# Kernel tuning notes

Measured on AMD Instinct MI355X. Metric: run time of the kernel, lower is better.

Reference implementation:

```python
import jax, jax.numpy as jnp
import numpy as np

PAD = 32      # person_attrs_dim
NZ = 64       # num_zones
T = 32768     # number of timesteps
D = PAD + 1 + NZ  # 97, input dim to the MLP


def _ln(x, g, b, eps=1e-5):
    # LayerNorm over the last (only) axis of a 1-D vector
    m = jnp.mean(x)
    v = jnp.mean((x - m) ** 2)
    return g * (x - m) / jnp.sqrt(v + eps) + b


def setup_inputs() -> dict:
    key = jax.random.key(0)
    ks = jax.random.split(key, 24)

    def xav(k, shape):  # xavier_normal_ for nn.Linear weight [out, in]
        std = np.sqrt(2.0 / (shape[0] + shape[1])).astype(np.float32)
        return std * jax.random.normal(k, shape, dtype=jnp.float32)

    def lng(k, n):  # layernorm gain (perturbed from 1 so grads are non-trivial)
        return 1.0 + 0.1 * jax.random.normal(k, (n,), dtype=jnp.float32)

    def lnb(k, n):
        return 0.1 * jax.random.normal(k, (n,), dtype=jnp.float32)

    inp = {
        "person_attrs": jax.random.normal(ks[0], (PAD,), dtype=jnp.float32),
        "times": jax.random.uniform(ks[1], (T,), dtype=jnp.float32) * 24.0,
        "zone_features": jax.random.normal(ks[2], (NZ, 16), dtype=jnp.float32),
        "edge_index": jax.random.randint(ks[3], (2, 256), 0, NZ, dtype=jnp.int32),
        # input_norm
        "g0": lng(ks[4], D), "b0": lnb(ks[5], D),
        # encoder1: Linear(D,256) + LN(256)
        "W1": xav(ks[6], (256, D)), "b1": jnp.zeros((256,), jnp.float32),
        "g1": lng(ks[7], 256), "be1": lnb(ks[8], 256),
        # encoder2: Linear(256,128) + LN(128)
        "W2": xav(ks[9], (128, 256)), "b2": jnp.zeros((128,), jnp.float32),
        "g2": lng(ks[10], 128), "be2": lnb(ks[11], 128),
        # output_layer: Linear(128,64) + LN(64) + Linear(64,NZ)
        "W3": xav(ks[12], (64, 128)), "b3": jnp.zeros((64,), jnp.float32),
        "g3": lng(ks[13], 64), "be3": lnb(ks[14], 64),
        "W4": xav(ks[15], (NZ, 64)), "b4": jnp.zeros((NZ,), jnp.float32),
    }
    return inp


def reference(person_attrs, times, zone_features, edge_index,
              g0, b0, W1, b1, g1, be1, W2, b2, g2, be2,
              W3, b3, g3, be3, W4, b4):
    nz = W4.shape[0]
    # set_graph_data: symmetric adjacency with self-loops (zone_features unused)
    u, v = edge_index[0], edge_index[1]
    A = jnp.zeros((nz, nz), jnp.float32).at[u, v].set(1.0).at[v, u].set(1.0)
    A = jnp.maximum(A, jnp.eye(nz, dtype=jnp.float32))

    def step(zone, t):
        onehot = jax.nn.one_hot(zone, nz, dtype=jnp.float32)
        x = jnp.concatenate([person_attrs, t[None], onehot])  # [D]
        x = _ln(x, g0, b0)
        h = jax.nn.relu(_ln(W1 @ x + b1, g1, be1))   # dropout is eval-mode identity
        h = jax.nn.relu(_ln(W2 @ h + b2, g2, be2))
        h = jax.nn.relu(_ln(W3 @ h + b3, g3, be3))
        raw = W4 @ h + b4                            # [nz] raw logits
        row = A[zone]
        # (raw/temp with invalid=-50/temp) * temp  ==  where(valid, raw, -50)
        pred = jnp.where(row > 0, raw, jnp.float32(-50.0))
        nxt = jnp.argmax(jnp.where(row > 0, raw, -jnp.inf)).astype(zone.dtype)
        return nxt, pred

    _, zone_logits = jax.lax.scan(step, jnp.array(0, jnp.int32), times)
    return zone_logits  # [T, nz]
```

## Files before the change

### kernel.cpp

```cpp
#include <hip/hip_runtime.h>
#include <stdint.h>

typedef __attribute__((ext_vector_type(8))) short bf16x8;
typedef __attribute__((ext_vector_type(4))) float f32x4;
typedef __attribute__((ext_vector_type(4))) unsigned int u32x4;

#define MFMA(a, b, c) __builtin_amdgcn_mfma_f32_16x16x32_bf16(a, b, c, 0, 0, 0)

__device__ __forceinline__ unsigned short f2b(float x) {
  unsigned u = __float_as_uint(x);
  return (unsigned short)((u + 0x7fffu + ((u >> 16) & 1u)) >> 16);
}
__device__ __forceinline__ float b2f(unsigned short h) {
  return __uint_as_float(((unsigned)h) << 16);
}

struct u2 { unsigned hi, lo; };
__device__ __forceinline__ u2 split2(float h0, float h1) {
  unsigned u0 = __float_as_uint(h0), u1 = __float_as_uint(h1);
  u2 r;
  r.hi = (u0 >> 16) | (u1 & 0xffff0000u);
  float r0 = h0 - __uint_as_float(u0 & 0xffff0000u);
  float r1 = h1 - __uint_as_float(u1 & 0xffff0000u);
  r.lo = (__float_as_uint(r0) >> 16) | (__float_as_uint(r1) & 0xffff0000u);
  return r;
}

#define SWZ(row, col) ((col) ^ ((((row) >> 2) & 1) << 4) ^ ((((row) >> 3) & 1) << 2))


__global__ void k_prep(const float* __restrict__ pa, const float* __restrict__ g0,
                       const float* __restrict__ b0, const float* __restrict__ W1,
                       const float* __restrict__ b1,
                       float* __restrict__ c_pa, float* __restrict__ w_t,
                       float* __restrict__ c_g, float* __restrict__ c_const,
                       float* __restrict__ scal, float* __restrict__ wzT,
                       float* __restrict__ wzZ) {
  int j = threadIdx.x;
  const float* wr = W1 + j * 97;
  float cg = 0.f, cc = 0.f, cp = 0.f;
  for (int k = 0; k < 97; ++k) { float w = wr[k]; cg += w * g0[k]; cc += w * b0[k]; }
  for (int k = 0; k < 32; ++k) cp += wr[k] * g0[k] * pa[k];
  c_g[j] = cg;
  c_const[j] = cc + b1[j];
  c_pa[j] = cp;
  w_t[j] = wr[32] * g0[32];
  for (int z = 0; z < 64; ++z) {
    float v = wr[33 + z] * g0[33 + z];
    wzT[j * 64 + z] = v;
    wzZ[z * 256 + j] = v;
  }
  if (j == 0) {
    float s = 0.f, q = 0.f;
    for (int k = 0; k < 32; ++k) { float x = pa[k]; s += x; q += x * x; }
    scal[0] = s; scal[1] = q;
  }
}

__global__ void k_prep2(const float* __restrict__ c_pa, const float* __restrict__ w_t,
                        const float* __restrict__ c_g, const float* __restrict__ c_const,
                        const float* __restrict__ wzT, float* __restrict__ st) {
  int tid = threadIdx.x;
  if (tid < 64) {
    int z = tid;
    float A = 0.f, Q = 0.f, dpa = 0.f, dwt = 0.f, dcg = 0.f, dcc = 0.f;
    for (int k = 0; k < 256; ++k) {
      float wz = wzT[k * 64 + z];
      A += wz; Q = fmaf(wz, wz, Q);
      dpa = fmaf(c_pa[k], wz, dpa);
      dwt = fmaf(w_t[k], wz, dwt);
      dcg = fmaf(c_g[k], wz, dcg);
      dcc = fmaf(c_const[k], wz, dcc);
    }
    st[z] = A; st[64 + z] = Q; st[128 + z] = dpa;
    st[192 + z] = dwt; st[256 + z] = dcg; st[320 + z] = dcc;
  } else {
    int lane = tid - 64;
    float acc[14];
    #pragma unroll
    for (int m = 0; m < 14; ++m) acc[m] = 0.f;
    for (int k = lane; k < 256; k += 64) {
      float P = c_pa[k], W = w_t[k], G = c_g[k], C = c_const[k];
      acc[0] += P; acc[1] += W; acc[2] += G; acc[3] += C;
      acc[4] = fmaf(P, P, acc[4]); acc[5] = fmaf(P, W, acc[5]);
      acc[6] = fmaf(P, G, acc[6]); acc[7] = fmaf(P, C, acc[7]);
      acc[8] = fmaf(W, W, acc[8]); acc[9] = fmaf(W, G, acc[9]);
      acc[10] = fmaf(W, C, acc[10]); acc[11] = fmaf(G, G, acc[11]);
      acc[12] = fmaf(G, C, acc[12]); acc[13] = fmaf(C, C, acc[13]);
    }
    #pragma unroll
    for (int off = 1; off < 64; off <<= 1) {
      #pragma unroll
      for (int m = 0; m < 14; ++m) acc[m] += __shfl_xor(acc[m], off, 64);
    }
    if (lane == 0) {
      #pragma unroll
      for (int m = 0; m < 14; ++m) st[386 + m] = acc[m];
    }
  }
}

__global__ void k_scal2st(const float* __restrict__ scal, float* __restrict__ st) {
  if (threadIdx.x < 2) st[384 + threadIdx.x] = scal[threadIdx.x];
}

__global__ void k_adj(const int* __restrict__ ei, unsigned long long* __restrict__ adj) {
  int t = threadIdx.x;
  if (t < 64) adj[t] = 1ull << t;
  __syncthreads();
  int u = ei[t] & 63, v = ei[256 + t] & 63;
  atomicOr(&adj[u], 1ull << v);
  atomicOr(&adj[v], 1ull << u);
}

__global__ void k_wsplit(const float* __restrict__ W2, const float* __restrict__ W3,
                         const float* __restrict__ W4,
                         unsigned short* __restrict__ W2Ah, unsigned short* __restrict__ W2Al,
                         unsigned short* __restrict__ W3Ah, unsigned short* __restrict__ W3Al,
                         unsigned short* __restrict__ W4Ah, unsigned short* __restrict__ W4Al) {
  int idx = blockIdx.x * 256 + threadIdx.x;
  float w; unsigned short* ph; unsigned short* pl; int o;
  if (idx < 32768) {
    int mt = idx >> 12, kt = (idx >> 9) & 7, lane = (idx >> 3) & 63, j = idx & 7;
    int m = mt * 16 + (lane & 15), k = kt * 32 + (lane >> 4) * 8 + j;
    w = W2[m * 256 + k]; ph = W2Ah; pl = W2Al; o = idx;
  } else if (idx < 40960) {
    int r = idx - 32768;
    int mt = r >> 11, kt = (r >> 9) & 3, lane = (r >> 3) & 63, j = r & 7;
    int m = mt * 16 + (lane & 15), k = kt * 32 + (lane >> 4) * 8 + j;
    w = W3[m * 128 + k]; ph = W3Ah; pl = W3Al; o = r;
  } else if (idx < 45056) {
    int r = idx - 40960;
    int mt = r >> 10, kt = (r >> 9) & 1, lane = (r >> 3) & 63, j = r & 7;
    int m = mt * 16 + (lane & 15), k = kt * 32 + (lane >> 4) * 8 + j;
    w = W4[m * 64 + k]; ph = W4Ah; pl = W4Al; o = r;
  } else return;
  unsigned short hb = f2b(w);
  ph[o] = hb;
  pl[o] = f2b(w - b2f(hb));
}


__global__ __launch_bounds__(256, 4) void k_pass1(
    const float* __restrict__ times,
    const float* __restrict__ c_pa, const float* __restrict__ w_t,
    const float* __restrict__ c_g, const float* __restrict__ c_const,
    const float* __restrict__ wzT, const float* __restrict__ st,
    const unsigned short* __restrict__ W2Ah, const unsigned short* __restrict__ W2Al,
    const unsigned short* __restrict__ W3Ah, const unsigned short* __restrict__ W3Al,
    const unsigned short* __restrict__ W4Ah, const unsigned short* __restrict__ W4Al,
    const float* __restrict__ b2, const float* __restrict__ b3,
    const float* __restrict__ b4,
    const float* __restrict__ g1, const float* __restrict__ be1,
    const float* __restrict__ g2, const float* __restrict__ be2,
    const float* __restrict__ g3, const float* __restrict__ be3,
    const unsigned long long* __restrict__ adj,
    unsigned char* __restrict__ nxt) {
  __shared__ __align__(16) char region[32768];
  __shared__ float u_lds[256];
  __shared__ float ps1[256], ps2[256];
  __shared__ unsigned long long pk[256];

  unsigned short* B1hi = (unsigned short*)region;
  unsigned short* B1lo = (unsigned short*)(region + 16384);
  float* h2p = (float*)region;
  unsigned short* B2hi = (unsigned short*)region;
  unsigned short* B2lo = (unsigned short*)(region + 16384);
  float* h3p = (float*)region;
  unsigned short* B3hi = (unsigned short*)(region + 16384);
  unsigned short* B3lo = (unsigned short*)(region + 24576);

  const int tid = threadIdx.x;
  const int lane = tid & 63;
  const int l15 = lane & 15;
  const int lhi = lane >> 4;
  const int w = __builtin_amdgcn_readfirstlane(tid >> 6);
  const int i = blockIdx.x;

  const float t = times[i];
  const float m0 = (st[384] + t + 1.0f) * (1.0f / 97.0f);
  const float e2 = (st[385] + t * t + 1.0f) * (1.0f / 97.0f);
  const float alpha = 1.0f / sqrtf(e2 - m0 * m0 + 1e-5f);
  const float gma = -m0 * alpha;

  const f32x4 zero4 = {0.f, 0.f, 0.f, 0.f};

  {
    int k = tid;
    float u = fmaf(t, w_t[k], c_pa[k]);
    u = fmaf(alpha, u, c_const[k]);
    u = fmaf(gma, c_g[k], u);
    u_lds[k] = u;
    float su = u, sq = u * u;
    #pragma unroll
    for (int off = 1; off < 64; off <<= 1) {
      su += __shfl_xor(su, off, 64);
      sq += __shfl_xor(sq, off, 64);
    }
    if (lane == 0) { ps1[w] = su; ps2[w] = sq; }
  }
  __syncthreads();
  float mu1, inv1;
  {
    float U1 = ps1[0] + ps1[1] + ps1[2] + ps1[3];
    float Qu = ps2[0] + ps2[1] + ps2[2] + ps2[3];
    float A1 = st[lane], Qz = st[64 + lane];
    float dpa = st[128 + lane], dwt = st[192 + lane];
    float dcg = st[256 + lane], dcc = st[320 + lane];
    float s1 = fmaf(alpha, A1, U1);
    float uwz = fmaf(alpha, fmaf(t, dwt, dpa), fmaf(gma, dcg, dcc));
    float s2 = Qu + 2.0f * alpha * uwz + alpha * alpha * Qz;
    mu1 = s1 * (1.0f / 256.0f);
    inv1 = 1.0f / sqrtf(s2 * (1.0f / 256.0f) - mu1 * mu1 + 1e-5f);
  }

  f32x4 acc[2][4];
  #pragma unroll
  for (int a = 0; a < 2; ++a)
    #pragma unroll
    for (int b = 0; b < 4; ++b) acc[a][b] = zero4;

  for (int kc = 0; kc < 2; ++kc) {
    if (kc) __syncthreads();
    #pragma unroll
    for (int q = 0; q < 4; ++q) {
      int kb = kc * 128 + w * 32 + q * 8;
      f32x4 u0 = *(const f32x4*)(u_lds + kb);
      f32x4 u1 = *(const f32x4*)(u_lds + kb + 4);
      float hbuf[8];
      #pragma unroll
      for (int j = 0; j < 8; ++j) {
        int k = kb + j;
        float u = (j < 4) ? u0[j] : u1[j - 4];
        float p = fmaf(alpha, wzT[k * 64 + lane], u);
        float gi = g1[k] * inv1;
        float bb = fmaf(-mu1, gi, be1[k]);
        hbuf[j] = fmaxf(fmaf(p, gi, bb), 0.f);
      }
      u32x4 vh, vl;
      #pragma unroll
      for (int e = 0; e < 4; ++e) {
        u2 s = split2(hbuf[2 * e], hbuf[2 * e + 1]);
        vh[e] = s.hi; vl[e] = s.lo;
      }
      int slotd = ((w * 4 + lhi) * 64 + q * 16 + l15) * 4;
      *(u32x4*)((unsigned*)B1hi + slotd) = vh;
      *(u32x4*)((unsigned*)B1lo + slotd) = vl;
    }
    __syncthreads();
    for (int kt = 0; kt < 4; ++kt) {
      int ktg = kc * 4 + kt;
      bf16x8 a0h = *(const bf16x8*)(W2Ah + (((2 * w + 0) * 8 + ktg) * 64 + lane) * 8);
      bf16x8 a0l = *(const bf16x8*)(W2Al + (((2 * w + 0) * 8 + ktg) * 64 + lane) * 8);
      bf16x8 a1h = *(const bf16x8*)(W2Ah + (((2 * w + 1) * 8 + ktg) * 64 + lane) * 8);
      bf16x8 a1l = *(const bf16x8*)(W2Al + (((2 * w + 1) * 8 + ktg) * 64 + lane) * 8);
      #pragma unroll
      for (int nt = 0; nt < 4; ++nt) {
        bf16x8 bh = *(const bf16x8*)(B1hi + ((kt * 4 + nt) * 64 + lane) * 8);
        bf16x8 bl = *(const bf16x8*)(B1lo + ((kt * 4 + nt) * 64 + lane) * 8);
        acc[0][nt] = MFMA(a0h, bh, acc[0][nt]);
        acc[0][nt] = MFMA(a0h, bl, acc[0][nt]);
        acc[0][nt] = MFMA(a0l, bh, acc[0][nt]);
        acc[1][nt] = MFMA(a1h, bh, acc[1][nt]);
        acc[1][nt] = MFMA(a1h, bl, acc[1][nt]);
        acc[1][nt] = MFMA(a1l, bh, acc[1][nt]);
      }
    }
  }
  #pragma unroll
  for (int mti = 0; mti < 2; ++mti) {
    f32x4 bv = *(const f32x4*)(b2 + w * 32 + mti * 16 + lhi * 4);
    #pragma unroll
    for (int nt = 0; nt < 4; ++nt) acc[mti][nt] += bv;
  }
  {
    float sa[4], sb[4];
    #pragma unroll
    for (int nt = 0; nt < 4; ++nt) {
      float x1 = 0.f, x2 = 0.f;
      #pragma unroll
      for (int mti = 0; mti < 2; ++mti)
        #pragma unroll
        for (int r = 0; r < 4; ++r) { float v = acc[mti][nt][r]; x1 += v; x2 += v * v; }
      x1 += __shfl_xor(x1, 16, 64); x1 += __shfl_xor(x1, 32, 64);
      x2 += __shfl_xor(x2, 16, 64); x2 += __shfl_xor(x2, 32, 64);
      sa[nt] = x1; sb[nt] = x2;
    }
    if (lane < 16) {
      #pragma unroll
      for (int nt = 0; nt < 4; ++nt) {
        ps1[w * 64 + nt * 16 + lane] = sa[nt];
        ps2[w * 64 + nt * 16 + lane] = sb[nt];
      }
    }
  }
  __syncthreads();
  #pragma unroll
  for (int mti = 0; mti < 2; ++mti)
    #pragma unroll
    for (int nt = 0; nt < 4; ++nt)
      #pragma unroll
      for (int r = 0; r < 4; ++r) {
        int row = w * 32 + mti * 16 + lhi * 4 + r;
        h2p[row * 64 + SWZ(row, nt * 16 + l15)] = acc[mti][nt][r];
      }
  __syncthreads();

  float mu2, inv2;
  {
    float a = ps1[lane] + ps1[64 + lane] + ps1[128 + lane] + ps1[192 + lane];
    float b = ps2[lane] + ps2[64 + lane] + ps2[128 + lane] + ps2[192 + lane];
    mu2 = a * (1.0f / 128.0f);
    inv2 = 1.0f / sqrtf(b * (1.0f / 128.0f) - mu2 * mu2 + 1e-5f);
  }
  float hv[32];
  #pragma unroll
  for (int mi = 0; mi < 32; ++mi) {
    int row = w * 32 + mi;
    hv[mi] = h2p[row * 64 + SWZ(row, lane)];
  }
  __syncthreads();
  #pragma unroll
  for (int q = 0; q < 4; ++q) {
    float hbuf[8];
    #pragma unroll
    for (int j = 0; j < 8; ++j) {
      int mi = q * 8 + j, mm = w * 32 + mi;
      float gi = g2[mm] * inv2;
      float bb = fmaf(-mu2, gi, be2[mm]);
      hbuf[j] = fmaxf(fmaf(hv[mi], gi, bb), 0.f);
    }
    u32x4 vh, vl;
    #pragma unroll
    for (int e = 0; e < 4; ++e) {
      u2 s = split2(hbuf[2 * e], hbuf[2 * e + 1]);
      vh[e] = s.hi; vl[e] = s.lo;
    }
    int slotd = ((w * 4 + lhi) * 64 + q * 16 + l15) * 4;
    *(u32x4*)((unsigned*)B2hi + slotd) = vh;
    *(u32x4*)((unsigned*)B2lo + slotd) = vl;
  }
  __syncthreads();

  f32x4 acc2[4];
  #pragma unroll
  for (int b = 0; b < 4; ++b) acc2[b] = zero4;
  for (int kt = 0; kt < 4; ++kt) {
    bf16x8 ah = *(const bf16x8*)(W3Ah + ((w * 4 + kt) * 64 + lane) * 8);
    bf16x8 al = *(const bf16x8*)(W3Al + ((w * 4 + kt) * 64 + lane) * 8);
    #pragma unroll
    for (int nt = 0; nt < 4; ++nt) {
      bf16x8 bh = *(const bf16x8*)(B2hi + ((kt * 4 + nt) * 64 + lane) * 8);
      bf16x8 bl = *(const bf16x8*)(B2lo + ((kt * 4 + nt) * 64 + lane) * 8);
      acc2[nt] = MFMA(ah, bh, acc2[nt]);
      acc2[nt] = MFMA(ah, bl, acc2[nt]);
      acc2[nt] = MFMA(al, bh, acc2[nt]);
    }
  }
  {
    f32x4 bv = *(const f32x4*)(b3 + w * 16 + lhi * 4);
    #pragma unroll
    for (int nt = 0; nt < 4; ++nt) acc2[nt] += bv;
  }
  {
    float sa[4], sb[4];
    #pragma unroll
    for (int nt = 0; nt < 4; ++nt) {
      float x1 = 0.f, x2 = 0.f;
      #pragma unroll
      for (int r = 0; r < 4; ++r) { float v = acc2[nt][r]; x1 += v; x2 += v * v; }
      x1 += __shfl_xor(x1, 16, 64); x1 += __shfl_xor(x1, 32, 64);
      x2 += __shfl_xor(x2, 16, 64); x2 += __shfl_xor(x2, 32, 64);
      sa[nt] = x1; sb[nt] = x2;
    }
    if (lane < 16) {
      #pragma unroll
      for (int nt = 0; nt < 4; ++nt) {
        ps1[w * 64 + nt * 16 + lane] = sa[nt];
        ps2[w * 64 + nt * 16 + lane] = sb[nt];
      }
    }
  }
  __syncthreads();
  #pragma unroll
  for (int nt = 0; nt < 4; ++nt)
    #pragma unroll
    for (int r = 0; r < 4; ++r) {
      int row = w * 16 + lhi * 4 + r;
      h3p[row * 64 + SWZ(row, nt * 16 + l15)] = acc2[nt][r];
    }
  __syncthreads();

  float mu3, inv3;
  {
    float a = ps1[lane] + ps1[64 + lane] + ps1[128 + lane] + ps1[192 + lane];
    float b = ps2[lane] + ps2[64 + lane] + ps2[128 + lane] + ps2[192 + lane];
    mu3 = a * (1.0f / 64.0f);
    inv3 = 1.0f / sqrtf(b * (1.0f / 64.0f) - mu3 * mu3 + 1e-5f);
  }
  #pragma unroll
  for (int q = 0; q < 2; ++q) {
    int o = w * 2 + q;
    float hbuf[8];
    #pragma unroll
    for (int j = 0; j < 8; ++j) {
      int mm = o * 8 + j;
      float v = h3p[mm * 64 + SWZ(mm, lane)];
      float gi = g3[mm] * inv3;
      float bb = fmaf(-mu3, gi, be3[mm]);
      hbuf[j] = fmaxf(fmaf(v, gi, bb), 0.f);
    }
    u32x4 vh, vl;
    #pragma unroll
    for (int e = 0; e < 4; ++e) {
      u2 s = split2(hbuf[2 * e], hbuf[2 * e + 1]);
      vh[e] = s.hi; vl[e] = s.lo;
    }
    int slotd = (((o >> 2) * 4 + lhi) * 64 + (o & 3) * 16 + l15) * 4;
    *(u32x4*)((unsigned*)B3hi + slotd) = vh;
    *(u32x4*)((unsigned*)B3lo + slotd) = vl;
  }
  __syncthreads();

  f32x4 acc3[4];
  #pragma unroll
  for (int b = 0; b < 4; ++b) acc3[b] = zero4;
  for (int kt = 0; kt < 2; ++kt) {
    bf16x8 ah = *(const bf16x8*)(W4Ah + ((w * 2 + kt) * 64 + lane) * 8);
    bf16x8 al = *(const bf16x8*)(W4Al + ((w * 2 + kt) * 64 + lane) * 8);
    #pragma unroll
    for (int nt = 0; nt < 4; ++nt) {
      bf16x8 bh = *(const bf16x8*)(B3hi + ((kt * 4 + nt) * 64 + lane) * 8);
      bf16x8 bl = *(const bf16x8*)(B3lo + ((kt * 4 + nt) * 64 + lane) * 8);
      acc3[nt] = MFMA(ah, bh, acc3[nt]);
      acc3[nt] = MFMA(ah, bl, acc3[nt]);
      acc3[nt] = MFMA(al, bh, acc3[nt]);
    }
  }
  f32x4 b4v = *(const f32x4*)(b4 + w * 16 + lhi * 4);
  unsigned long long kbest[4];
  #pragma unroll
  for (int nt = 0; nt < 4; ++nt) {
    unsigned long long am = adj[nt * 16 + l15];
    unsigned long long kb = 0ull;
    #pragma unroll
    for (int r = 0; r < 4; ++r) {
      int o = w * 16 + lhi * 4 + r;
      float raw = acc3[nt][r] + b4v[r];
      float val = ((am >> o) & 1ull) ? raw : -__builtin_huge_valf();
      unsigned u = __float_as_uint(val);
      u = (u & 0x80000000u) ? ~u : (u | 0x80000000u);
      unsigned long long key = ((unsigned long long)u << 6) | (unsigned long long)(63 - o);
      if (key > kb) kb = key;
    }
    unsigned long long oth = __shfl_xor(kb, 16, 64); if (oth > kb) kb = oth;
    oth = __shfl_xor(kb, 32, 64); if (oth > kb) kb = oth;
    kbest[nt] = kb;
  }
  if (lane < 16) {
    #pragma unroll
    for (int nt = 0; nt < 4; ++nt) pk[w * 64 + nt * 16 + lane] = kbest[nt];
  }
  __syncthreads();
  if (tid < 64) {
    unsigned long long k0 = pk[tid], k1 = pk[64 + tid];
    unsigned long long k2 = pk[128 + tid], k3 = pk[192 + tid];
    unsigned long long a = k0 > k1 ? k0 : k1;
    unsigned long long b = k2 > k3 ? k2 : k3;
    unsigned long long bb = a > b ? a : b;
    nxt[(size_t)i * 64 + tid] = (unsigned char)(63u - (unsigned)(bb & 63ull));
  }
}


__global__ void k_scan_a(const unsigned char* __restrict__ nxt,
                         unsigned char* __restrict__ cmap) {
  int c = blockIdx.x, lane = threadIdx.x;
  int g = lane;
  const unsigned char* p = nxt + (size_t)c * 128 * 64;
  for (int s = 0; s < 128; ++s) {
    int sig = p[s * 64 + lane];
    g = __shfl(sig, g, 64);
  }
  cmap[c * 64 + lane] = (unsigned char)g;
}

__global__ void k_scan_b(const unsigned char* __restrict__ cmap,
                         int* __restrict__ startz) {
  int lane = threadIdx.x;
  int cur = 0;
  for (int c = 0; c < 256; ++c) {
    if (lane == 0) startz[c] = cur;
    int row = cmap[c * 64 + lane];
    cur = __shfl(row, cur, 64);
  }
}

__global__ void k_scan_c(const unsigned char* __restrict__ nxt,
                         const int* __restrict__ startz,
                         unsigned char* __restrict__ zones) {
  int c = blockIdx.x, lane = threadIdx.x;
  int cur = startz[c];
  const unsigned char* p = nxt + (size_t)c * 128 * 64;
  for (int s = 0; s < 128; ++s) {
    if (lane == 0) zones[c * 128 + s] = (unsigned char)cur;
    int row = p[s * 64 + lane];
    cur = __shfl(row, cur, 64);
  }
}


__global__ __launch_bounds__(256, 2) void k_pass2m(
    const float* __restrict__ times, const unsigned char* __restrict__ zones,
    const float* __restrict__ c_pa, const float* __restrict__ w_t,
    const float* __restrict__ c_g, const float* __restrict__ c_const,
    const float* __restrict__ wzZ, const float* __restrict__ st,
    const unsigned short* __restrict__ W2Ah, const unsigned short* __restrict__ W2Al,
    const unsigned short* __restrict__ W3Ah, const unsigned short* __restrict__ W3Al,
    const unsigned short* __restrict__ W4Ah, const unsigned short* __restrict__ W4Al,
    const float* __restrict__ b2, const float* __restrict__ b3,
    const float* __restrict__ b4,
    const float* __restrict__ g1, const float* __restrict__ be1,
    const float* __restrict__ g2, const float* __restrict__ be2,
    const float* __restrict__ g3, const float* __restrict__ be3,
    const unsigned long long* __restrict__ adj,
    float* __restrict__ out) {
  __shared__ __align__(16) char region[32768];
  __shared__ float ps1[256], ps2[256];
  __shared__ unsigned long long am_lds[64];

  unsigned short* B1hi = (unsigned short*)region;
  unsigned short* B1lo = (unsigned short*)(region + 16384);
  float* h2p = (float*)region;
  unsigned short* B2hi = (unsigned short*)region;
  unsigned short* B2lo = (unsigned short*)(region + 16384);
  float* h3p = (float*)region;
  unsigned short* B3hi = (unsigned short*)(region + 16384);
  unsigned short* B3lo = (unsigned short*)(region + 24576);
  float* outT = (float*)region;

  const int tid = threadIdx.x;
  const int lane = tid & 63;
  const int l15 = lane & 15;
  const int lhi = lane >> 4;
  const int w = __builtin_amdgcn_readfirstlane(tid >> 6);
  const int i0 = blockIdx.x * 64;

  const float t = times[i0 + lane];
  const int z = zones[i0 + lane];
  const int zrow = z << 8;
  if (tid < 64) am_lds[tid] = adj[zones[i0 + tid]];

  const float m0 = (st[384] + t + 1.0f) * (1.0f / 97.0f);
  const float e2 = (st[385] + t * t + 1.0f) * (1.0f / 97.0f);
  const float a0 = 1.0f / sqrtf(e2 - m0 * m0 + 1e-5f);
  const float a1 = a0 * t;
  const float a2 = -m0 * a0;

  float mu1, inv1;
  {
    float SP = st[386], SW = st[387], SG = st[388], SC = st[389];
    float PP = st[390], PW = st[391], PG = st[392], PC = st[393];
    float WW = st[394], WG = st[395], WC = st[396];
    float GG = st[397], GC = st[398], CC = st[399];
    float U1 = a0 * SP + a1 * SW + a2 * SG + SC;
    float s1 = fmaf(a0, st[z], U1);
    float Qu = a0 * a0 * PP + a1 * a1 * WW + a2 * a2 * GG + CC
             + 2.0f * (a0 * a1 * PW + a0 * a2 * PG + a0 * PC
                       + a1 * a2 * WG + a1 * WC + a2 * GC);
    float uwz = a0 * st[128 + z] + a1 * st[192 + z] + a2 * st[256 + z] + st[320 + z];
    float s2 = Qu + 2.0f * a0 * uwz + a0 * a0 * st[64 + z];
    mu1 = s1 * (1.0f / 256.0f);
    inv1 = 1.0f / sqrtf(s2 * (1.0f / 256.0f) - mu1 * mu1 + 1e-5f);
  }

  const f32x4 zero4 = {0.f, 0.f, 0.f, 0.f};
  f32x4 acc[2][4];
  #pragma unroll
  for (int a = 0; a < 2; ++a)
    #pragma unroll
    for (int b = 0; b < 4; ++b) acc[a][b] = zero4;

  for (int kc = 0; kc < 2; ++kc) {
    if (kc) __syncthreads();
    #pragma unroll
    for (int q = 0; q < 4; ++q) {
      int kb = kc * 128 + w * 32 + q * 8;
      float hbuf[8];
      #pragma unroll
      for (int j = 0; j < 8; ++j) {
        int k = kb + j;
        float u = fmaf(a0, c_pa[k], fmaf(a1, w_t[k], fmaf(a2, c_g[k], c_const[k])));
        float p = fmaf(a0, wzZ[zrow + k], u);
        float gi = g1[k] * inv1;
        float bb = fmaf(-mu1, gi, be1[k]);
        hbuf[j] = fmaxf(fmaf(p, gi, bb), 0.f);
      }
      u32x4 vh, vl;
      #pragma unroll
      for (int e = 0; e < 4; ++e) {
        u2 s = split2(hbuf[2 * e], hbuf[2 * e + 1]);
        vh[e] = s.hi; vl[e] = s.lo;
      }
      int slotd = ((w * 4 + lhi) * 64 + q * 16 + l15) * 4;
      *(u32x4*)((unsigned*)B1hi + slotd) = vh;
      *(u32x4*)((unsigned*)B1lo + slotd) = vl;
    }
    __syncthreads();
    for (int kt = 0; kt < 4; ++kt) {
      int ktg = kc * 4 + kt;
      bf16x8 a0h = *(const bf16x8*)(W2Ah + (((2 * w + 0) * 8 + ktg) * 64 + lane) * 8);
      bf16x8 a0l = *(const bf16x8*)(W2Al + (((2 * w + 0) * 8 + ktg) * 64 + lane) * 8);
      bf16x8 a1h = *(const bf16x8*)(W2Ah + (((2 * w + 1) * 8 + ktg) * 64 + lane) * 8);
      bf16x8 a1l = *(const bf16x8*)(W2Al + (((2 * w + 1) * 8 + ktg) * 64 + lane) * 8);
      #pragma unroll
      for (int nt = 0; nt < 4; ++nt) {
        bf16x8 bh = *(const bf16x8*)(B1hi + ((kt * 4 + nt) * 64 + lane) * 8);
        bf16x8 bl = *(const bf16x8*)(B1lo + ((kt * 4 + nt) * 64 + lane) * 8);
        acc[0][nt] = MFMA(a0h, bh, acc[0][nt]);
        acc[0][nt] = MFMA(a0h, bl, acc[0][nt]);
        acc[0][nt] = MFMA(a0l, bh, acc[0][nt]);
        acc[1][nt] = MFMA(a1h, bh, acc[1][nt]);
        acc[1][nt] = MFMA(a1h, bl, acc[1][nt]);
        acc[1][nt] = MFMA(a1l, bh, acc[1][nt]);
      }
    }
  }
  #pragma unroll
  for (int mti = 0; mti < 2; ++mti) {
    f32x4 bv = *(const f32x4*)(b2 + w * 32 + mti * 16 + lhi * 4);
    #pragma unroll
    for (int nt = 0; nt < 4; ++nt) acc[mti][nt] += bv;
  }
  {
    float sa[4], sb[4];
    #pragma unroll
    for (int nt = 0; nt < 4; ++nt) {
      float x1 = 0.f, x2 = 0.f;
      #pragma unroll
      for (int mti = 0; mti < 2; ++mti)
        #pragma unroll
        for (int r = 0; r < 4; ++r) { float v = acc[mti][nt][r]; x1 += v; x2 += v * v; }
      x1 += __shfl_xor(x1, 16, 64); x1 += __shfl_xor(x1, 32, 64);
      x2 += __shfl_xor(x2, 16, 64); x2 += __shfl_xor(x2, 32, 64);
      sa[nt] = x1; sb[nt] = x2;
    }
    if (lane < 16) {
      #pragma unroll
      for (int nt = 0; nt < 4; ++nt) {
        ps1[w * 64 + nt * 16 + lane] = sa[nt];
        ps2[w * 64 + nt * 16 + lane] = sb[nt];
      }
    }
  }
  __syncthreads();
  #pragma unroll
  for (int mti = 0; mti < 2; ++mti)
    #pragma unroll
    for (int nt = 0; nt < 4; ++nt)
      #pragma unroll
      for (int r = 0; r < 4; ++r) {
        int row = w * 32 + mti * 16 + lhi * 4 + r;
        h2p[row * 64 + SWZ(row, nt * 16 + l15)] = acc[mti][nt][r];
      }
  __syncthreads();

  float mu2, inv2;
  {
    float a = ps1[lane] + ps1[64 + lane] + ps1[128 + lane] + ps1[192 + lane];
    float b = ps2[lane] + ps2[64 + lane] + ps2[128 + lane] + ps2[192 + lane];
    mu2 = a * (1.0f / 128.0f);
    inv2 = 1.0f / sqrtf(b * (1.0f / 128.0f) - mu2 * mu2 + 1e-5f);
  }
  float hv[32];
  #pragma unroll
  for (int mi = 0; mi < 32; ++mi) {
    int row = w * 32 + mi;
    hv[mi] = h2p[row * 64 + SWZ(row, lane)];
  }
  __syncthreads();
  #pragma unroll
  for (int q = 0; q < 4; ++q) {
    float hbuf[8];
    #pragma unroll
    for (int j = 0; j < 8; ++j) {
      int mi = q * 8 + j, mm = w * 32 + mi;
      float gi = g2[mm] * inv2;
      float bb = fmaf(-mu2, gi, be2[mm]);
      hbuf[j] = fmaxf(fmaf(hv[mi], gi, bb), 0.f);
    }
    u32x4 vh, vl;
    #pragma unroll
    for (int e = 0; e < 4; ++e) {
      u2 s = split2(hbuf[2 * e], hbuf[2 * e + 1]);
      vh[e] = s.hi; vl[e] = s.lo;
    }
    int slotd = ((w * 4 + lhi) * 64 + q * 16 + l15) * 4;
    *(u32x4*)((unsigned*)B2hi + slotd) = vh;
    *(u32x4*)((unsigned*)B2lo + slotd) = vl;
  }
  __syncthreads();

  f32x4 acc2[4];
  #pragma unroll
  for (int b = 0; b < 4; ++b) acc2[b] = zero4;
  for (int kt = 0; kt < 4; ++kt) {
    bf16x8 ah = *(const bf16x8*)(W3Ah + ((w * 4 + kt) * 64 + lane) * 8);
    bf16x8 al = *(const bf16x8*)(W3Al + ((w * 4 + kt) * 64 + lane) * 8);
    #pragma unroll
    for (int nt = 0; nt < 4; ++nt) {
      bf16x8 bh = *(const bf16x8*)(B2hi + ((kt * 4 + nt) * 64 + lane) * 8);
      bf16x8 bl = *(const bf16x8*)(B2lo + ((kt * 4 + nt) * 64 + lane) * 8);
      acc2[nt] = MFMA(ah, bh, acc2[nt]);
      acc2[nt] = MFMA(ah, bl, acc2[nt]);
      acc2[nt] = MFMA(al, bh, acc2[nt]);
    }
  }
  {
    f32x4 bv = *(const f32x4*)(b3 + w * 16 + lhi * 4);
    #pragma unroll
    for (int nt = 0; nt < 4; ++nt) acc2[nt] += bv;
  }
  {
    float sa[4], sb[4];
    #pragma unroll
    for (int nt = 0; nt < 4; ++nt) {
      float x1 = 0.f, x2 = 0.f;
      #pragma unroll
      for (int r = 0; r < 4; ++r) { float v = acc2[nt][r]; x1 += v; x2 += v * v; }
      x1 += __shfl_xor(x1, 16, 64); x1 += __shfl_xor(x1, 32, 64);
      x2 += __shfl_xor(x2, 16, 64); x2 += __shfl_xor(x2, 32, 64);
      sa[nt] = x1; sb[nt] = x2;
    }
    if (lane < 16) {
      #pragma unroll
      for (int nt = 0; nt < 4; ++nt) {
        ps1[w * 64 + nt * 16 + lane] = sa[nt];
        ps2[w * 64 + nt * 16 + lane] = sb[nt];
      }
    }
  }
  __syncthreads();
  #pragma unroll
  for (int nt = 0; nt < 4; ++nt)
    #pragma unroll
    for (int r = 0; r < 4; ++r) {
      int row = w * 16 + lhi * 4 + r;
      h3p[row * 64 + SWZ(row, nt * 16 + l15)] = acc2[nt][r];
    }
  __syncthreads();

  float mu3, inv3;
  {
    float a = ps1[lane] + ps1[64 + lane] + ps1[128 + lane] + ps1[192 + lane];
    float b = ps2[lane] + ps2[64 + lane] + ps2[128 + lane] + ps2[192 + lane];
    mu3 = a * (1.0f / 64.0f);
    inv3 = 1.0f / sqrtf(b * (1.0f / 64.0f) - mu3 * mu3 + 1e-5f);
  }
  #pragma unroll
  for (int q = 0; q < 2; ++q) {
    int o = w * 2 + q;
    float hbuf[8];
    #pragma unroll
    for (int j = 0; j < 8; ++j) {
      int mm = o * 8 + j;
      float v = h3p[mm * 64 + SWZ(mm, lane)];
      float gi = g3[mm] * inv3;
      float bb = fmaf(-mu3, gi, be3[mm]);
      hbuf[j] = fmaxf(fmaf(v, gi, bb), 0.f);
    }
    u32x4 vh, vl;
    #pragma unroll
    for (int e = 0; e < 4; ++e) {
      u2 s = split2(hbuf[2 * e], hbuf[2 * e + 1]);
      vh[e] = s.hi; vl[e] = s.lo;
    }
    int slotd = (((o >> 2) * 4 + lhi) * 64 + (o & 3) * 16 + l15) * 4;
    *(u32x4*)((unsigned*)B3hi + slotd) = vh;
    *(u32x4*)((unsigned*)B3lo + slotd) = vl;
  }
  __syncthreads();

  f32x4 acc3[4];
  #pragma unroll
  for (int b = 0; b < 4; ++b) acc3[b] = zero4;
  for (int kt = 0; kt < 2; ++kt) {
    bf16x8 ah = *(const bf16x8*)(W4Ah + ((w * 2 + kt) * 64 + lane) * 8);
    bf16x8 al = *(const bf16x8*)(W4Al + ((w * 2 + kt) * 64 + lane) * 8);
    #pragma unroll
    for (int nt = 0; nt < 4; ++nt) {
      bf16x8 bh = *(const bf16x8*)(B3hi + ((kt * 4 + nt) * 64 + lane) * 8);
      bf16x8 bl = *(const bf16x8*)(B3lo + ((kt * 4 + nt) * 64 + lane) * 8);
      acc3[nt] = MFMA(ah, bh, acc3[nt]);
      acc3[nt] = MFMA(ah, bl, acc3[nt]);
      acc3[nt] = MFMA(al, bh, acc3[nt]);
    }
  }
  f32x4 b4v = *(const f32x4*)(b4 + w * 16 + lhi * 4);
  #pragma unroll
  for (int nt = 0; nt < 4; ++nt) {
    unsigned long long am = am_lds[nt * 16 + l15];
    #pragma unroll
    for (int r = 0; r < 4; ++r) {
      int o = w * 16 + lhi * 4 + r;
      float raw = acc3[nt][r] + b4v[r];
      float predv = ((am >> o) & 1ull) ? raw : -50.0f;
      int b = nt * 16 + l15;
      outT[b * 64 + SWZ(b, o)] = predv;
    }
  }
  __syncthreads();
  {
    int b = tid >> 2, cb = (tid & 3) * 16;
    size_t gbase = ((size_t)(i0 + b)) * 64 + cb;
    #pragma unroll
    for (int c4 = 0; c4 < 4; ++c4) {
      int col = cb + c4 * 4;
      f32x4 v = *(const f32x4*)(outT + b * 64 + SWZ(b, col));
      *(f32x4*)(out + gbase + c4 * 4) = v;
    }
  }
}


extern "C" void kernel_launch(void* const* d_in, const int* in_sizes, int n_in,
                              void* d_out, int out_size, void* d_ws, size_t ws_size,
                              hipStream_t stream) {
  const float* pa    = (const float*)d_in[0];
  const float* times = (const float*)d_in[1];
  const int*   ei    = (const int*)d_in[3];
  const float* g0    = (const float*)d_in[4];
  const float* b0    = (const float*)d_in[5];
  const float* W1    = (const float*)d_in[6];
  const float* b1    = (const float*)d_in[7];
  const float* g1    = (const float*)d_in[8];
  const float* be1   = (const float*)d_in[9];
  const float* W2    = (const float*)d_in[10];
  const float* b2    = (const float*)d_in[11];
  const float* g2    = (const float*)d_in[12];
  const float* be2   = (const float*)d_in[13];
  const float* W3    = (const float*)d_in[14];
  const float* b3    = (const float*)d_in[15];
  const float* g3    = (const float*)d_in[16];
  const float* be3   = (const float*)d_in[17];
  const float* W4    = (const float*)d_in[18];
  const float* b4    = (const float*)d_in[19];

  char* ws = (char*)d_ws;
  float* c_pa    = (float*)(ws + 0);
  float* w_t     = (float*)(ws + 1024);
  float* c_g     = (float*)(ws + 2048);
  float* c_const = (float*)(ws + 3072);
  float* scal    = (float*)(ws + 4096);
  unsigned long long* adj = (unsigned long long*)(ws + 4608);
  float* wzT = (float*)(ws + 5120);
  float* wzZ = (float*)(ws + 70656);
  unsigned short* W2Ah = (unsigned short*)(ws + 136192);
  unsigned short* W2Al = (unsigned short*)(ws + 201728);
  unsigned short* W3Ah = (unsigned short*)(ws + 267264);
  unsigned short* W3Al = (unsigned short*)(ws + 283648);
  unsigned short* W4Ah = (unsigned short*)(ws + 300032);
  unsigned short* W4Al = (unsigned short*)(ws + 308224);
  float* st = (float*)(ws + 316416);
  unsigned char* nxt  = (unsigned char*)(ws + 318464);
  unsigned char* cmap = (unsigned char*)(ws + 2415616);
  int* startz = (int*)(ws + 2432000);
  unsigned char* zones = (unsigned char*)(ws + 2433024);

  k_prep<<<1, 256, 0, stream>>>(pa, g0, b0, W1, b1, c_pa, w_t, c_g, c_const,
                                scal, wzT, wzZ);
  k_prep2<<<1, 128, 0, stream>>>(c_pa, w_t, c_g, c_const, wzT, st);
  k_scal2st<<<1, 64, 0, stream>>>(scal, st);
  k_adj<<<1, 256, 0, stream>>>(ei, adj);
  k_wsplit<<<176, 256, 0, stream>>>(W2, W3, W4, W2Ah, W2Al, W3Ah, W3Al, W4Ah, W4Al);
  k_pass1<<<32768, 256, 0, stream>>>(times, c_pa, w_t, c_g, c_const, wzT, st,
                                     W2Ah, W2Al, W3Ah, W3Al, W4Ah, W4Al,
                                     b2, b3, b4, g1, be1, g2, be2, g3, be3,
                                     adj, nxt);
  k_scan_a<<<256, 64, 0, stream>>>(nxt, cmap);
  k_scan_b<<<1, 64, 0, stream>>>(cmap, startz);
  k_scan_c<<<256, 64, 0, stream>>>(nxt, startz, zones);
  k_pass2m<<<512, 256, 0, stream>>>(times, zones, c_pa, w_t, c_g, c_const,
                                    wzZ, st, W2Ah, W2Al, W3Ah, W3Al, W4Ah, W4Al,
                                    b2, b3, b4, g1, be1, g2, be2, g3, be3,
                                    adj, (float*)d_out);
}
```

Baseline: 809.2 us.

## Apply LayerNorm directly on MFMA accumulators and precompute second K-chunk before GEMM

Layers 2 and 3 previously stored pre-norm activations to LDS in row layout, re-read them transposed, normalized, then packed them into the B-operand layout. The new code computes per-column mean and variance from the partial sums and normalizes in registers, writing the hi/lo bf16 split straight into the next layer's B-fragment layout. This removes an LDS round trip and two barriers per layer. The layer-1 activations for the second K chunk are now computed before the first chunk's MFMAs so their math can overlap the matrix work, at the cost of more live registers and a changed LDS buffer layout.

```diff
diff --git a/kernel.cpp b/kernel.cpp
--- a/kernel.cpp
+++ b/kernel.cpp
@@ -4,6 +4,7 @@
 typedef __attribute__((ext_vector_type(8))) short bf16x8;
 typedef __attribute__((ext_vector_type(4))) float f32x4;
 typedef __attribute__((ext_vector_type(4))) unsigned int u32x4;
+typedef __attribute__((ext_vector_type(2))) unsigned int u32x2;
 
 #define MFMA(a, b, c) __builtin_amdgcn_mfma_f32_16x16x32_bf16(a, b, c, 0, 0, 0)
 
@@ -158,17 +159,15 @@
     unsigned char* __restrict__ nxt) {
   __shared__ __align__(16) char region[32768];
   __shared__ float u_lds[256];
-  __shared__ float ps1[256], ps2[256];
-  __shared__ unsigned long long pk[256];
+  __shared__ float ps[512];
 
   unsigned short* B1hi = (unsigned short*)region;
   unsigned short* B1lo = (unsigned short*)(region + 16384);
-  float* h2p = (float*)region;
   unsigned short* B2hi = (unsigned short*)region;
   unsigned short* B2lo = (unsigned short*)(region + 16384);
-  float* h3p = (float*)region;
-  unsigned short* B3hi = (unsigned short*)(region + 16384);
-  unsigned short* B3lo = (unsigned short*)(region + 24576);
+  unsigned short* B3hi = (unsigned short*)region;
+  unsigned short* B3lo = (unsigned short*)(region + 8192);
+  unsigned long long* pk = (unsigned long long*)ps;
 
   const int tid = threadIdx.x;
   const int lane = tid & 63;
@@ -197,13 +196,13 @@
       su += __shfl_xor(su, off, 64);
       sq += __shfl_xor(sq, off, 64);
     }
-    if (lane == 0) { ps1[w] = su; ps2[w] = sq; }
+    if (lane == 0) { ps[w] = su; ps[256 + w] = sq; }
   }
   __syncthreads();
   float mu1, inv1;
   {
-    float U1 = ps1[0] + ps1[1] + ps1[2] + ps1[3];
-    float Qu = ps2[0] + ps2[1] + ps2[2] + ps2[3];
+    float U1 = ps[0] + ps[1] + ps[2] + ps[3];
+    float Qu = ps[256] + ps[257] + ps[258] + ps[259];
     float A1 = st[lane], Qz = st[64 + lane];
     float dpa = st[128 + lane], dwt = st[192 + lane];
     float dcg = st[256 + lane], dcc = st[320 + lane];
@@ -220,53 +219,102 @@
     #pragma unroll
     for (int b = 0; b < 4; ++b) acc[a][b] = zero4;
 
-  for (int kc = 0; kc < 2; ++kc) {
-    if (kc) __syncthreads();
-    #pragma unroll
-    for (int q = 0; q < 4; ++q) {
-      int kb = kc * 128 + w * 32 + q * 8;
-      f32x4 u0 = *(const f32x4*)(u_lds + kb);
-      f32x4 u1 = *(const f32x4*)(u_lds + kb + 4);
-      float hbuf[8];
-      #pragma unroll
-      for (int j = 0; j < 8; ++j) {
-        int k = kb + j;
-        float u = (j < 4) ? u0[j] : u1[j - 4];
-        float p = fmaf(alpha, wzT[k * 64 + lane], u);
-        float gi = g1[k] * inv1;
-        float bb = fmaf(-mu1, gi, be1[k]);
-        hbuf[j] = fmaxf(fmaf(p, gi, bb), 0.f);
-      }
-      u32x4 vh, vl;
-      #pragma unroll
-      for (int e = 0; e < 4; ++e) {
-        u2 s = split2(hbuf[2 * e], hbuf[2 * e + 1]);
-        vh[e] = s.hi; vl[e] = s.lo;
-      }
-      int slotd = ((w * 4 + lhi) * 64 + q * 16 + l15) * 4;
-      *(u32x4*)((unsigned*)B1hi + slotd) = vh;
-      *(u32x4*)((unsigned*)B1lo + slotd) = vl;
-    }
-    __syncthreads();
-    for (int kt = 0; kt < 4; ++kt) {
-      int ktg = kc * 4 + kt;
-      bf16x8 a0h = *(const bf16x8*)(W2Ah + (((2 * w + 0) * 8 + ktg) * 64 + lane) * 8);
-      bf16x8 a0l = *(const bf16x8*)(W2Al + (((2 * w + 0) * 8 + ktg) * 64 + lane) * 8);
-      bf16x8 a1h = *(const bf16x8*)(W2Ah + (((2 * w + 1) * 8 + ktg) * 64 + lane) * 8);
-      bf16x8 a1l = *(const bf16x8*)(W2Al + (((2 * w + 1) * 8 + ktg) * 64 + lane) * 8);
-      #pragma unroll
-      for (int nt = 0; nt < 4; ++nt) {
-        bf16x8 bh = *(const bf16x8*)(B1hi + ((kt * 4 + nt) * 64 + lane) * 8);
-        bf16x8 bl = *(const bf16x8*)(B1lo + ((kt * 4 + nt) * 64 + lane) * 8);
-        acc[0][nt] = MFMA(a0h, bh, acc[0][nt]);
-        acc[0][nt] = MFMA(a0h, bl, acc[0][nt]);
-        acc[0][nt] = MFMA(a0l, bh, acc[0][nt]);
-        acc[1][nt] = MFMA(a1h, bh, acc[1][nt]);
-        acc[1][nt] = MFMA(a1h, bl, acc[1][nt]);
-        acc[1][nt] = MFMA(a1l, bh, acc[1][nt]);
-      }
-    }
-  }
+  u32x4 hh[4], hl[4];
+
+  #pragma unroll
+  for (int q = 0; q < 4; ++q) {
+    int kb = w * 32 + q * 8;
+    f32x4 u0 = *(const f32x4*)(u_lds + kb);
+    f32x4 u1v = *(const f32x4*)(u_lds + kb + 4);
+    float hbuf[8];
+    #pragma unroll
+    for (int j = 0; j < 8; ++j) {
+      int k = kb + j;
+      float u = (j < 4) ? u0[j] : u1v[j - 4];
+      float p = fmaf(alpha, wzT[k * 64 + lane], u);
+      float gi = g1[k] * inv1;
+      float bb = fmaf(-mu1, gi, be1[k]);
+      hbuf[j] = fmaxf(fmaf(p, gi, bb), 0.f);
+    }
+    #pragma unroll
+    for (int e = 0; e < 4; ++e) {
+      u2 s = split2(hbuf[2 * e], hbuf[2 * e + 1]);
+      hh[q][e] = s.hi; hl[q][e] = s.lo;
+    }
+  }
+  #pragma unroll
+  for (int q = 0; q < 4; ++q) {
+    int slotd = ((w * 4 + lhi) * 64 + q * 16 + l15) * 4;
+    *(u32x4*)((unsigned*)B1hi + slotd) = hh[q];
+    *(u32x4*)((unsigned*)B1lo + slotd) = hl[q];
+  }
+  __syncthreads();
+
+  #pragma unroll
+  for (int q = 0; q < 4; ++q) {
+    int kb = 128 + w * 32 + q * 8;
+    f32x4 u0 = *(const f32x4*)(u_lds + kb);
+    f32x4 u1v = *(const f32x4*)(u_lds + kb + 4);
+    float hbuf[8];
+    #pragma unroll
+    for (int j = 0; j < 8; ++j) {
+      int k = kb + j;
+      float u = (j < 4) ? u0[j] : u1v[j - 4];
+      float p = fmaf(alpha, wzT[k * 64 + lane], u);
+      float gi = g1[k] * inv1;
+      float bb = fmaf(-mu1, gi, be1[k]);
+      hbuf[j] = fmaxf(fmaf(p, gi, bb), 0.f);
+    }
+    #pragma unroll
+    for (int e = 0; e < 4; ++e) {
+      u2 s = split2(hbuf[2 * e], hbuf[2 * e + 1]);
+      hh[q][e] = s.hi; hl[q][e] = s.lo;
+    }
+  }
+  for (int kt = 0; kt < 4; ++kt) {
+    bf16x8 a0h = *(const bf16x8*)(W2Ah + (((2 * w + 0) * 8 + kt) * 64 + lane) * 8);
+    bf16x8 a0l = *(const bf16x8*)(W2Al + (((2 * w + 0) * 8 + kt) * 64 + lane) * 8);
+    bf16x8 a1h = *(const bf16x8*)(W2Ah + (((2 * w + 1) * 8 + kt) * 64 + lane) * 8);
+    bf16x8 a1l = *(const bf16x8*)(W2Al + (((2 * w + 1) * 8 + kt) * 64 + lane) * 8);
+    #pragma unroll
+    for (int nt = 0; nt < 4; ++nt) {
+      bf16x8 bh = *(const bf16x8*)(B1hi + ((kt * 4 + nt) * 64 + lane) * 8);
+      bf16x8 bl = *(const bf16x8*)(B1lo + ((kt * 4 + nt) * 64 + lane) * 8);
+      acc[0][nt] = MFMA(a0h, bh, acc[0][nt]);
+      acc[0][nt] = MFMA(a0h, bl, acc[0][nt]);
+      acc[0][nt] = MFMA(a0l, bh, acc[0][nt]);
+      acc[1][nt] = MFMA(a1h, bh, acc[1][nt]);
+      acc[1][nt] = MFMA(a1h, bl, acc[1][nt]);
+      acc[1][nt] = MFMA(a1l, bh, acc[1][nt]);
+    }
+  }
+  __syncthreads();
+  #pragma unroll
+  for (int q = 0; q < 4; ++q) {
+    int slotd = ((w * 4 + lhi) * 64 + q * 16 + l15) * 4;
+    *(u32x4*)((unsigned*)B1hi + slotd) = hh[q];
+    *(u32x4*)((unsigned*)B1lo + slotd) = hl[q];
+  }
+  __syncthreads();
+  for (int kt = 0; kt < 4; ++kt) {
+    int ktg = 4 + kt;
+    bf16x8 a0h = *(const bf16x8*)(W2Ah + (((2 * w + 0) * 8 + ktg) * 64 + lane) * 8);
+    bf16x8 a0l = *(const bf16x8*)(W2Al + (((2 * w + 0) * 8 + ktg) * 64 + lane) * 8);
+    bf16x8 a1h = *(const bf16x8*)(W2Ah + (((2 * w + 1) * 8 + ktg) * 64 + lane) * 8);
+    bf16x8 a1l = *(const bf16x8*)(W2Al + (((2 * w + 1) * 8 + ktg) * 64 + lane) * 8);
+    #pragma unroll
+    for (int nt = 0; nt < 4; ++nt) {
+      bf16x8 bh = *(const bf16x8*)(B1hi + ((kt * 4 + nt) * 64 + lane) * 8);
+      bf16x8 bl = *(const bf16x8*)(B1lo + ((kt * 4 + nt) * 64 + lane) * 8);
+      acc[0][nt] = MFMA(a0h, bh, acc[0][nt]);
+      acc[0][nt] = MFMA(a0h, bl, acc[0][nt]);
+      acc[0][nt] = MFMA(a0l, bh, acc[0][nt]);
+      acc[1][nt] = MFMA(a1h, bh, acc[1][nt]);
+      acc[1][nt] = MFMA(a1h, bl, acc[1][nt]);
+      acc[1][nt] = MFMA(a1l, bh, acc[1][nt]);
+    }
+  }
+
   #pragma unroll
   for (int mti = 0; mti < 2; ++mti) {
     f32x4 bv = *(const f32x4*)(b2 + w * 32 + mti * 16 + lhi * 4);
@@ -274,7 +322,6 @@
     for (int nt = 0; nt < 4; ++nt) acc[mti][nt] += bv;
   }
   {
-    float sa[4], sb[4];
     #pragma unroll
     for (int nt = 0; nt < 4; ++nt) {
       float x1 = 0.f, x2 = 0.f;
@@ -284,61 +331,50 @@
         for (int r = 0; r < 4; ++r) { float v = acc[mti][nt][r]; x1 += v; x2 += v * v; }
       x1 += __shfl_xor(x1, 16, 64); x1 += __shfl_xor(x1, 32, 64);
       x2 += __shfl_xor(x2, 16, 64); x2 += __shfl_xor(x2, 32, 64);
-      sa[nt] = x1; sb[nt] = x2;
-    }
-    if (lane < 16) {
+      if (lane < 16) {
+        ps[w * 64 + nt * 16 + lane] = x1;
+        ps[256 + w * 64 + nt * 16 + lane] = x2;
+      }
+    }
+  }
+  __syncthreads();
+
+  {
+    float mu2v[4], iv2v[4];
+    #pragma unroll
+    for (int nt = 0; nt < 4; ++nt) {
+      int c = nt * 16 + l15;
+      float a = ps[c] + ps[64 + c] + ps[128 + c] + ps[192 + c];
+      float b = ps[256 + c] + ps[320 + c] + ps[384 + c] + ps[448 + c];
+      mu2v[nt] = a * (1.0f / 128.0f);
+      iv2v[nt] = 1.0f / sqrtf(b * (1.0f / 128.0f) - mu2v[nt] * mu2v[nt] + 1e-5f);
+    }
+    f32x4 g2v[2], be2v[2];
+    #pragma unroll
+    for (int mti = 0; mti < 2; ++mti) {
+      g2v[mti]  = *(const f32x4*)(g2  + w * 32 + mti * 16 + lhi * 4);
+      be2v[mti] = *(const f32x4*)(be2 + w * 32 + mti * 16 + lhi * 4);
+    }
+    #pragma unroll
+    for (int mti = 0; mti < 2; ++mti)
       #pragma unroll
       for (int nt = 0; nt < 4; ++nt) {
-        ps1[w * 64 + nt * 16 + lane] = sa[nt];
-        ps2[w * 64 + nt * 16 + lane] = sb[nt];
+        float h[4];
+        #pragma unroll
+        for (int r = 0; r < 4; ++r) {
+          float G = g2v[mti][r] * iv2v[nt];
+          float B = fmaf(-mu2v[nt], G, be2v[mti][r]);
+          h[r] = fmaxf(fmaf(acc[mti][nt][r], G, B), 0.f);
+        }
+        u2 s01 = split2(h[0], h[1]);
+        u2 s23 = split2(h[2], h[3]);
+        int base = ((w * 4 + nt) * 64 + (2 * mti + (lhi >> 1)) * 16 + l15) * 8
+                 + 4 * (lhi & 1);
+        u32x2 vh = {s01.hi, s23.hi};
+        u32x2 vl = {s01.lo, s23.lo};
+        *(u32x2*)(B2hi + base) = vh;
+        *(u32x2*)(B2lo + base) = vl;
       }
-    }
-  }
-  __syncthreads();
-  #pragma unroll
-  for (int mti = 0; mti < 2; ++mti)
-    #pragma unroll
-    for (int nt = 0; nt < 4; ++nt)
-      #pragma unroll
-      for (int r = 0; r < 4; ++r) {
-        int row = w * 32 + mti * 16 + lhi * 4 + r;
-        h2p[row * 64 + SWZ(row, nt * 16 + l15)] = acc[mti][nt][r];
-      }
-  __syncthreads();
-
-  float mu2, inv2;
-  {
-    float a = ps1[lane] + ps1[64 + lane] + ps1[128 + lane] + ps1[192 + lane];
-    float b = ps2[lane] + ps2[64 + lane] + ps2[128 + lane] + ps2[192 + lane];
-    mu2 = a * (1.0f / 128.0f);
-    inv2 = 1.0f / sqrtf(b * (1.0f / 128.0f) - mu2 * mu2 + 1e-5f);
-  }
-  float hv[32];
-  #pragma unroll
-  for (int mi = 0; mi < 32; ++mi) {
-    int row = w * 32 + mi;
-    hv[mi] = h2p[row * 64 + SWZ(row, lane)];
-  }
-  __syncthreads();
-  #pragma unroll
-  for (int q = 0; q < 4; ++q) {
-    float hbuf[8];
-    #pragma unroll
-    for (int j = 0; j < 8; ++j) {
-      int mi = q * 8 + j, mm = w * 32 + mi;
-      float gi = g2[mm] * inv2;
-      float bb = fmaf(-mu2, gi, be2[mm]);
-      hbuf[j] = fmaxf(fmaf(hv[mi], gi, bb), 0.f);
-    }
-    u32x4 vh, vl;
-    #pragma unroll
-    for (int e = 0; e < 4; ++e) {
-      u2 s = split2(hbuf[2 * e], hbuf[2 * e + 1]);
-      vh[e] = s.hi; vl[e] = s.lo;
-    }
-    int slotd = ((w * 4 + lhi) * 64 + q * 16 + l15) * 4;
-    *(u32x4*)((unsigned*)B2hi + slotd) = vh;
-    *(u32x4*)((unsigned*)B2lo + slotd) = vl;
   }
   __syncthreads();
 
@@ -363,7 +399,6 @@
     for (int nt = 0; nt < 4; ++nt) acc2[nt] += bv;
   }
   {
-    float sa[4], sb[4];
     #pragma unroll
     for (int nt = 0; nt < 4; ++nt) {
       float x1 = 0.f, x2 = 0.f;
@@ -371,54 +406,44 @@
       for (int r = 0; r < 4; ++r) { float v = acc2[nt][r]; x1 += v; x2 += v * v; }
       x1 += __shfl_xor(x1, 16, 64); x1 += __shfl_xor(x1, 32, 64);
       x2 += __shfl_xor(x2, 16, 64); x2 += __shfl_xor(x2, 32, 64);
-      sa[nt] = x1; sb[nt] = x2;
-    }
-    if (lane < 16) {
-      #pragma unroll
-      for (int nt = 0; nt < 4; ++nt) {
-        ps1[w * 64 + nt * 16 + lane] = sa[nt];
-        ps2[w * 64 + nt * 16 + lane] = sb[nt];
+      if (lane < 16) {
+        ps[w * 64 + nt * 16 + lane] = x1;
+        ps[256 + w * 64 + nt * 16 + lane] = x2;
       }
     }
   }
   __syncthreads();
-  #pragma unroll
-  for (int nt = 0; nt < 4; ++nt)
-    #pragma unroll
-    for (int r = 0; r < 4; ++r) {
-      int row = w * 16 + lhi * 4 + r;
-      h3p[row * 64 + SWZ(row, nt * 16 + l15)] = acc2[nt][r];
-    }
-  __syncthreads();
-
-  float mu3, inv3;
-  {
-    float a = ps1[lane] + ps1[64 + lane] + ps1[128 + lane] + ps1[192 + lane];
-    float b = ps2[lane] + ps2[64 + lane] + ps2[128 + lane] + ps2[192 + lane];
-    mu3 = a * (1.0f / 64.0f);
-    inv3 = 1.0f / sqrtf(b * (1.0f / 64.0f) - mu3 * mu3 + 1e-5f);
-  }
-  #pragma unroll
-  for (int q = 0; q < 2; ++q) {
-    int o = w * 2 + q;
-    float hbuf[8];
-    #pragma unroll
-    for (int j = 0; j < 8; ++j) {
-      int mm = o * 8 + j;
-      float v = h3p[mm * 64 + SWZ(mm, lane)];
-      float gi = g3[mm] * inv3;
-      float bb = fmaf(-mu3, gi, be3[mm]);
-      hbuf[j] = fmaxf(fmaf(v, gi, bb), 0.f);
-    }
-    u32x4 vh, vl;
-    #pragma unroll
-    for (int e = 0; e < 4; ++e) {
-      u2 s = split2(hbuf[2 * e], hbuf[2 * e + 1]);
-      vh[e] = s.hi; vl[e] = s.lo;
-    }
-    int slotd = (((o >> 2) * 4 + lhi) * 64 + (o & 3) * 16 + l15) * 4;
-    *(u32x4*)((unsigned*)B3hi + slotd) = vh;
-    *(u32x4*)((unsigned*)B3lo + slotd) = vl;
+
+  {
+    float mu3v[4], iv3v[4];
+    #pragma unroll
+    for (int nt = 0; nt < 4; ++nt) {
+      int c = nt * 16 + l15;
+      float a = ps[c] + ps[64 + c] + ps[128 + c] + ps[192 + c];
+      float b = ps[256 + c] + ps[320 + c] + ps[384 + c] + ps[448 + c];
+      mu3v[nt] = a * (1.0f / 64.0f);
+      iv3v[nt] = 1.0f / sqrtf(b * (1.0f / 64.0f) - mu3v[nt] * mu3v[nt] + 1e-5f);
+    }
+    f32x4 g3v  = *(const f32x4*)(g3  + w * 16 + lhi * 4);
+    f32x4 be3v = *(const f32x4*)(be3 + w * 16 + lhi * 4);
+    #pragma unroll
+    for (int nt = 0; nt < 4; ++nt) {
+      float h[4];
+      #pragma unroll
+      for (int r = 0; r < 4; ++r) {
+        float G = g3v[r] * iv3v[nt];
+        float B = fmaf(-mu3v[nt], G, be3v[r]);
+        h[r] = fmaxf(fmaf(acc2[nt][r], G, B), 0.f);
+      }
+      u2 s01 = split2(h[0], h[1]);
+      u2 s23 = split2(h[2], h[3]);
+      int base = (((w >> 1) * 4 + nt) * 64 + (2 * (w & 1) + (lhi >> 1)) * 16 + l15) * 8
+               + 4 * (lhi & 1);
+      u32x2 vh = {s01.hi, s23.hi};
+      u32x2 vl = {s01.lo, s23.lo};
+      *(u32x2*)(B3hi + base) = vh;
+      *(u32x2*)(B3lo + base) = vl;
+    }
   }
   __syncthreads();
 
```

After: 833.7 us. 3.0% more time.
